# Optimization experiments

Measured on AMD Instinct MI355X. Metric: run time of the kernel, lower is better.

The kernel has to match this reference:

```python
import jax, jax.numpy as jnp
import numpy as np

B, S, I, H = 128, 512, 256, 512

def setup_inputs() -> dict:
    key = jax.random.key(0)
    ks = jax.random.split(key, 8)
    s_wd = 1.0 / np.sqrt(H)
    s_u = 1.0 / np.sqrt(I)
    return {
        "inputs": jax.random.normal(ks[0], (B, S, I), dtype=jnp.float32),
        "timestamps": jax.random.uniform(ks[1], (B, S), dtype=jnp.float32),
        "W_all_w": jax.random.uniform(ks[2], (4 * H, H), minval=-s_wd, maxval=s_wd, dtype=jnp.float32),
        "W_all_b": jax.random.uniform(ks[3], (4 * H,), minval=-s_wd, maxval=s_wd, dtype=jnp.float32),
        "U_all_w": jax.random.uniform(ks[4], (4 * H, I), minval=-s_u, maxval=s_u, dtype=jnp.float32),
        "U_all_b": jax.random.uniform(ks[5], (4 * H,), minval=-s_u, maxval=s_u, dtype=jnp.float32),
        "W_d_w": jax.random.uniform(ks[6], (H, H), minval=-s_wd, maxval=s_wd, dtype=jnp.float32),
        "W_d_b": jax.random.uniform(ks[7], (H,), minval=-s_wd, maxval=s_wd, dtype=jnp.float32),
    }

def reference(inputs, timestamps, W_all_w, W_all_b, U_all_w, U_all_b, W_d_w, W_d_b):
    b, seq, _ = inputs.shape
    hdim = W_d_w.shape[0]
    # Precompute input projection for all steps: [b, s, 4H] -> scan over [s, b, 4H]
    u_all = jnp.einsum("bsi,gi->bsg", inputs, U_all_w) + U_all_b
    u_seq = jnp.swapaxes(u_all, 0, 1)          # [s, b, 4H]
    t_seq = jnp.swapaxes(timestamps, 0, 1)     # [s, b]

    def step(carry, xs):
        h, c = carry
        u, t = xs
        c_s1 = jnp.tanh(c @ W_d_w.T + W_d_b)
        c_adj = c - c_s1 + c_s1 * t[:, None]   # c_l + c_s2
        outs = h @ W_all_w.T + W_all_b + u
        f, i, o, c_tmp = jnp.split(outs, 4, axis=1)
        f = jax.nn.sigmoid(f)
        i = jax.nn.sigmoid(i)
        o = jax.nn.sigmoid(o)
        c_tmp = jax.nn.sigmoid(c_tmp)
        c_new = f * c_adj + i * c_tmp
        h_new = o * jnp.tanh(c_new)
        return (h_new, c_new), h_new

    h0 = jnp.zeros((b, hdim), dtype=inputs.dtype)
    c0 = jnp.zeros((b, hdim), dtype=inputs.dtype)
    _, outputs = jax.lax.scan(step, (h0, c0), (u_seq, t_seq))
    return jnp.swapaxes(outputs, 0, 1)         # [b, s, H]
```

## Files before the change

kernel.cpp:

```cpp
#include <hip/hip_runtime.h>


#define Bq 128
#define Sq 512
#define Iq 256
#define Hq 512

typedef __bf16  bf16x8  __attribute__((ext_vector_type(8)));
typedef float   floatx4 __attribute__((ext_vector_type(4)));
typedef unsigned short ushort;
typedef ushort  ushort8 __attribute__((ext_vector_type(8)));
typedef unsigned long long u64;

__device__ __forceinline__ ushort f2bf(float f) {
    union { float f; unsigned u; } v; v.f = f;
    unsigned r = v.u + 0x7fffu + ((v.u >> 16) & 1u);
    return (ushort)(r >> 16);
}

__device__ __forceinline__ float sigm(float x) { return 1.f / (1.f + __expf(-x)); }
__device__ __forceinline__ float tanh_fast(float x) {
    float e = __expf(2.f * x);
    return 1.f - 2.f / (e + 1.f);
}

__device__ __forceinline__ bf16x8 pack8(float4 a, float4 b) {
    ushort8 v;
    v[0] = f2bf(a.x); v[1] = f2bf(a.y); v[2] = f2bf(a.z); v[3] = f2bf(a.w);
    v[4] = f2bf(b.x); v[5] = f2bf(b.y); v[6] = f2bf(b.z); v[7] = f2bf(b.w);
    return __builtin_bit_cast(bf16x8, v);
}

__global__ __launch_bounds__(256, 1) void lstm_kernel(
    const float* __restrict__ xin,
    const float* __restrict__ tsp,
    const float* __restrict__ Ww, const float* __restrict__ Wb,
    const float* __restrict__ Uw, const float* __restrict__ Ub,
    const float* __restrict__ Dw, const float* __restrict__ Db,
    unsigned* __restrict__ hcbuf,
    unsigned* __restrict__ slots,
    float* __restrict__ out)
{
    __shared__ ushort h_s[16 * 520];
    __shared__ ushort c_s[16 * 520];
    __shared__ ushort x_s[16 * 264];
    __shared__ float  gb[4 * 256];
    __shared__ float  gd[4 * 256];
    __shared__ float  bias_g[64];
    __shared__ float  bias_d[16];

    const int tid  = threadIdx.x;
    const int lane = tid & 63;
    const int wv   = tid >> 6;
    const int n    = lane & 15;
    const int quad = lane >> 4;
    const int gq   = blockIdx.x & 7;
    const int s    = blockIdx.x >> 3;
    const int jj   = s * 16;

    bf16x8 bW[16], bU[8], bD[4];
    {
        const int Rw = wv * Hq + jj + n;
        #pragma unroll
        for (int kk = 0; kk < 16; ++kk) {
            const float4* p = (const float4*)(Ww + (size_t)Rw * Hq + kk * 32 + quad * 8);
            bW[kk] = pack8(p[0], p[1]);
        }
        #pragma unroll
        for (int kk = 0; kk < 8; ++kk) {
            const float4* p = (const float4*)(Uw + (size_t)Rw * Iq + kk * 32 + quad * 8);
            bU[kk] = pack8(p[0], p[1]);
        }
        const int Rd = jj + n;
        #pragma unroll
        for (int kq = 0; kq < 4; ++kq) {
            const float4* p = (const float4*)(Dw + (size_t)Rd * Hq + (wv * 4 + kq) * 32 + quad * 8);
            bD[kq] = pack8(p[0], p[1]);
        }
    }
    if (tid < 64)
        bias_g[tid] = Wb[(tid >> 4) * Hq + jj + (tid & 15)] + Ub[(tid >> 4) * Hq + jj + (tid & 15)];
    if (tid >= 64 && tid < 80)
        bias_d[tid - 64] = Db[jj + (tid - 64)];
    __syncthreads();

    float c_reg = 0.f;
    const int b = tid >> 4, j = tid & 15;
    const int grow = gq * 16 + b;

    const ushort* hp = &h_s[n * 520 + quad * 8];
    const ushort* cp = &c_s[n * 520 + quad * 8];
    const ushort* xp = &x_s[n * 264 + quad * 8];

    unsigned* myslot = &slots[gq * 64 + s];
    unsigned* pollp  = &slots[gq * 64 + (lane & 31)];

    const float* xbase = xin + ((size_t)(gq * 16 + (tid >> 4)) * Sq) * Iq + (tid & 15) * 16;
    float4 x0, x1, x2, x3;
    {
        const float4* p = (const float4*)xbase;
        x0 = p[0]; x1 = p[1]; x2 = p[2]; x3 = p[3];
    }

    for (int t = 0; t < Sq; ++t) {
        float tt = tsp[(size_t)grow * Sq + t];

        const u64* hsrc = (const u64*)(hcbuf + ((size_t)(t & 1) * 8 + gq) * 8192);
        const u64* csrc = hsrc + 2048;
        u64 hv[8], cv[8];
        #pragma unroll
        for (int k = 0; k < 8; ++k)
            hv[k] = __hip_atomic_load(hsrc + k * 256 + tid, __ATOMIC_RELAXED, __HIP_MEMORY_SCOPE_AGENT);
        #pragma unroll
        for (int k = 0; k < 8; ++k)
            cv[k] = __hip_atomic_load(csrc + k * 256 + tid, __ATOMIC_RELAXED, __HIP_MEMORY_SCOPE_AGENT);

        {
            bf16x8 v0 = pack8(x0, x1);
            bf16x8 v1 = pack8(x2, x3);
            ushort* xd = &x_s[(tid >> 4) * 264 + (tid & 15) * 16];
            *(bf16x8*)xd       = v0;
            *(bf16x8*)(xd + 8) = v1;
        }

        #pragma unroll
        for (int k = 0; k < 8; ++k) {
            const int m   = k * 256 + tid;
            const int row = m >> 7;
            const int col = (m << 2) & 511;
            *(u64*)&h_s[row * 520 + col] = hv[k];
            *(u64*)&c_s[row * 520 + col] = cv[k];
        }
        __syncthreads();

        floatx4 accW = {0.f, 0.f, 0.f, 0.f};
        floatx4 accU = {0.f, 0.f, 0.f, 0.f};
        floatx4 accD = {0.f, 0.f, 0.f, 0.f};
        #pragma unroll
        for (int kk = 0; kk < 16; ++kk) {
            bf16x8 ah = *(const bf16x8*)(hp + kk * 32);
            accW = __builtin_amdgcn_mfma_f32_16x16x32_bf16(ah, bW[kk], accW, 0, 0, 0);
            if (kk < 8) {
                bf16x8 ax = *(const bf16x8*)(xp + kk * 32);
                accU = __builtin_amdgcn_mfma_f32_16x16x32_bf16(ax, bU[kk], accU, 0, 0, 0);
            }
            if ((kk >> 2) == wv) {
                bf16x8 ac = *(const bf16x8*)(cp + kk * 32);
                accD = __builtin_amdgcn_mfma_f32_16x16x32_bf16(ac, bD[kk & 3], accD, 0, 0, 0);
            }
        }
        accW += accU;

        #pragma unroll
        for (int r2 = 0; r2 < 4; ++r2) {
            gb[wv * 256 + (quad * 4 + r2) * 16 + n] = accW[r2];
            gd[wv * 256 + (quad * 4 + r2) * 16 + n] = accD[r2];
        }
        __syncthreads();

        float pf = gb[tid]       + bias_g[j];
        float pi = gb[256 + tid] + bias_g[16 + j];
        float po = gb[512 + tid] + bias_g[32 + j];
        float pc = gb[768 + tid] + bias_g[48 + j];
        float csum = gd[tid] + gd[256 + tid] + gd[512 + tid] + gd[768 + tid] + bias_d[j];
        float c_s1  = tanh_fast(csum);
        float c_adj = c_reg - c_s1 + c_s1 * tt;
        float fg = sigm(pf), ig = sigm(pi), og = sigm(po), cg = sigm(pc);
        float c_new = fg * c_adj + ig * cg;
        float h_new = og * tanh_fast(c_new);
        c_reg = c_new;

        out[((size_t)grow * Sq + t) * Hq + jj + j] = h_new;

        {
            unsigned my    = ((unsigned)f2bf(c_new) << 16) | (unsigned)f2bf(h_new);
            unsigned other = __shfl_xor(my, 1);
            unsigned* dst  = hcbuf + ((size_t)((t + 1) & 1) * 8 + gq) * 8192;
            const int pidx = b * 256 + ((jj + j) >> 1);
            if ((j & 1) == 0) {
                unsigned hpair = ((other & 0xFFFFu) << 16) | (my & 0xFFFFu);
                __hip_atomic_store(dst + pidx, hpair, __ATOMIC_RELAXED, __HIP_MEMORY_SCOPE_AGENT);
            } else {
                unsigned cpair = (my & 0xFFFF0000u) | (other >> 16);
                __hip_atomic_store(dst + 4096 + pidx, cpair, __ATOMIC_RELAXED, __HIP_MEMORY_SCOPE_AGENT);
            }
        }
        __syncthreads();

        if (t < Sq - 1) {
            const unsigned tgt = (unsigned)(t + 1);
            if (tid == 0)
                __hip_atomic_store(myslot, tgt, __ATOMIC_RELAXED, __HIP_MEMORY_SCOPE_AGENT);

            {
                const float4* p = (const float4*)(xbase + (size_t)(t + 1) * Iq);
                x0 = p[0]; x1 = p[1]; x2 = p[2]; x3 = p[3];
            }

            if (wv == 0) {
                for (;;) {
                    unsigned vv = __hip_atomic_load(pollp, __ATOMIC_RELAXED, __HIP_MEMORY_SCOPE_AGENT);
                    if (__all(vv >= tgt)) break;
                    __builtin_amdgcn_s_sleep(2);
                }
            }
            __syncthreads();
        }
    }
}

extern "C" void kernel_launch(void* const* d_in, const int* in_sizes, int n_in,
                              void* d_out, int out_size, void* d_ws, size_t ws_size,
                              hipStream_t stream) {
    const float* inputs = (const float*)d_in[0];
    const float* tsp    = (const float*)d_in[1];
    const float* Ww     = (const float*)d_in[2];
    const float* Wb     = (const float*)d_in[3];
    const float* Uw     = (const float*)d_in[4];
    const float* Ub     = (const float*)d_in[5];
    const float* Dw     = (const float*)d_in[6];
    const float* Db     = (const float*)d_in[7];
    float* out = (float*)d_out;

    char* ws = (char*)d_ws;
    unsigned* hcbuf = (unsigned*)ws;
    unsigned* slots = (unsigned*)(ws + 524288);

    hipMemsetAsync(ws, 0, 262144, stream);
    hipMemsetAsync(ws + 524288, 0, 2048, stream);

    lstm_kernel<<<dim3(256), dim3(256), 0, stream>>>(
        inputs, tsp, Ww, Wb, Uw, Ub, Dw, Db, hcbuf, slots, out);
}
```

Baseline: 1.816 ms.

## Use XCC-local sc0 loads/stores for h/c exchange when group shares an XCD

At startup each block records its XCC id, and the 32 blocks of a batch group check whether they all sit on the same XCD. If they do, the per-step h/c state exchange uses global loads and stores with only the sc0 cache bit instead of agent-scope atomics, so traffic can stay in the shared L2 rather than going further out. An explicit s_waitcnt is added before the shared-memory writes. The fast path relies on the hardware scheduler placing a group on one XCD; the startup handshake adds a small cost, and the sc0 coherence assumptions are subtle.

Measured after the change: 1.854 ms. +2.1%, slower.

```diff
diff --git a/kernel.cpp b/kernel.cpp
--- a/kernel.cpp
+++ b/kernel.cpp
@@ -29,6 +29,15 @@
     v[0] = f2bf(a.x); v[1] = f2bf(a.y); v[2] = f2bf(a.z); v[3] = f2bf(a.w);
     v[4] = f2bf(b.x); v[5] = f2bf(b.y); v[6] = f2bf(b.z); v[7] = f2bf(b.w);
     return __builtin_bit_cast(bf16x8, v);
+}
+
+__device__ __forceinline__ u64 ld_sc0_b64(const u64* p) {
+    u64 r;
+    asm volatile("global_load_dwordx2 %0, %1, off sc0" : "=v"(r) : "v"(p) : "memory");
+    return r;
+}
+__device__ __forceinline__ void st_sc0_b32(unsigned* p, unsigned v) {
+    asm volatile("global_store_dword %0, %1, off sc0" :: "v"(p), "v"(v) : "memory");
 }
 
 __global__ __launch_bounds__(256, 1) void lstm_kernel(
@@ -48,6 +57,7 @@
     __shared__ float  gd[4 * 256];
     __shared__ float  bias_g[64];
     __shared__ float  bias_d[16];
+    __shared__ int    fastflag_s;
 
     const int tid  = threadIdx.x;
     const int lane = tid & 63;
@@ -82,7 +92,28 @@
         bias_g[tid] = Wb[(tid >> 4) * Hq + jj + (tid & 15)] + Ub[(tid >> 4) * Hq + jj + (tid & 15)];
     if (tid >= 64 && tid < 80)
         bias_d[tid - 64] = Db[jj + (tid - 64)];
-    __syncthreads();
+
+    {
+        int xcc;
+        asm volatile("s_getreg_b32 %0, hwreg(HW_REG_XCC_ID)" : "=s"(xcc));
+        if (tid == 0)
+            __hip_atomic_store(&slots[gq * 64 + 32 + s], (unsigned)(xcc + 1),
+                               __ATOMIC_RELAXED, __HIP_MEMORY_SCOPE_AGENT);
+        if (wv == 0) {
+            unsigned vv;
+            for (;;) {
+                vv = __hip_atomic_load(&slots[gq * 64 + 32 + (lane & 31)],
+                                       __ATOMIC_RELAXED, __HIP_MEMORY_SCOPE_AGENT);
+                if (__all(vv != 0)) break;
+                __builtin_amdgcn_s_sleep(2);
+            }
+            unsigned f0 = __shfl(vv, 0);
+            int alleq = __all(vv == f0);
+            if (lane == 0) fastflag_s = alleq;
+        }
+        __syncthreads();
+    }
+    const bool fastpath = (fastflag_s != 0);
 
     float c_reg = 0.f;
     const int b = tid >> 4, j = tid & 15;
@@ -108,12 +139,19 @@
         const u64* hsrc = (const u64*)(hcbuf + ((size_t)(t & 1) * 8 + gq) * 8192);
         const u64* csrc = hsrc + 2048;
         u64 hv[8], cv[8];
-        #pragma unroll
-        for (int k = 0; k < 8; ++k)
-            hv[k] = __hip_atomic_load(hsrc + k * 256 + tid, __ATOMIC_RELAXED, __HIP_MEMORY_SCOPE_AGENT);
-        #pragma unroll
-        for (int k = 0; k < 8; ++k)
-            cv[k] = __hip_atomic_load(csrc + k * 256 + tid, __ATOMIC_RELAXED, __HIP_MEMORY_SCOPE_AGENT);
+        if (fastpath) {
+            #pragma unroll
+            for (int k = 0; k < 8; ++k) hv[k] = ld_sc0_b64(hsrc + k * 256 + tid);
+            #pragma unroll
+            for (int k = 0; k < 8; ++k) cv[k] = ld_sc0_b64(csrc + k * 256 + tid);
+        } else {
+            #pragma unroll
+            for (int k = 0; k < 8; ++k)
+                hv[k] = __hip_atomic_load(hsrc + k * 256 + tid, __ATOMIC_RELAXED, __HIP_MEMORY_SCOPE_AGENT);
+            #pragma unroll
+            for (int k = 0; k < 8; ++k)
+                cv[k] = __hip_atomic_load(csrc + k * 256 + tid, __ATOMIC_RELAXED, __HIP_MEMORY_SCOPE_AGENT);
+        }
 
         {
             bf16x8 v0 = pack8(x0, x1);
@@ -121,6 +159,11 @@
             ushort* xd = &x_s[(tid >> 4) * 264 + (tid & 15) * 16];
             *(bf16x8*)xd       = v0;
             *(bf16x8*)(xd + 8) = v1;
+        }
+
+        if (fastpath) {
+            asm volatile("s_waitcnt vmcnt(0)" ::: "memory");
+            __builtin_amdgcn_sched_barrier(0);
         }
 
         #pragma unroll
@@ -177,13 +220,18 @@
             unsigned other = __shfl_xor(my, 1);
             unsigned* dst  = hcbuf + ((size_t)((t + 1) & 1) * 8 + gq) * 8192;
             const int pidx = b * 256 + ((jj + j) >> 1);
+            unsigned val; unsigned* ptr;
             if ((j & 1) == 0) {
-                unsigned hpair = ((other & 0xFFFFu) << 16) | (my & 0xFFFFu);
-                __hip_atomic_store(dst + pidx, hpair, __ATOMIC_RELAXED, __HIP_MEMORY_SCOPE_AGENT);
+                val = ((other & 0xFFFFu) << 16) | (my & 0xFFFFu);
+                ptr = dst + pidx;
             } else {
-                unsigned cpair = (my & 0xFFFF0000u) | (other >> 16);
-                __hip_atomic_store(dst + 4096 + pidx, cpair, __ATOMIC_RELAXED, __HIP_MEMORY_SCOPE_AGENT);
-            }
+                val = (my & 0xFFFF0000u) | (other >> 16);
+                ptr = dst + 4096 + pidx;
+            }
+            if (fastpath)
+                st_sc0_b32(ptr, val);
+            else
+                __hip_atomic_store(ptr, val, __ATOMIC_RELAXED, __HIP_MEMORY_SCOPE_AGENT);
         }
         __syncthreads();
 
```

## Split each batch group into two half-batches and ping-pong them to hide grid-sync latency

Applied to the files above, without the earlier changes.

Each block's 16 batch rows become two 8-row halves (A and B) that take turns through the recurrence. Each half has its own flags and h/c exchange buffers, so the wait on the other half's grid-wide flags overlaps the current half's MFMA and gate work. The inter-block barrier latency is meant to be hidden behind useful compute. In exchange the MFMA work per step doubles, since each pass still runs full 16-row tiles and discards half of them. Gate math now runs on only two waves while the other waves poll, and raw s_barrier plus waitcnt asm add correctness risk.

Result: slower. 2.636 ms (+45.2%).

```diff
diff --git a/kernel.cpp b/kernel.cpp
--- a/kernel.cpp
+++ b/kernel.cpp
@@ -29,6 +29,12 @@
     v[0] = f2bf(a.x); v[1] = f2bf(a.y); v[2] = f2bf(a.z); v[3] = f2bf(a.w);
     v[4] = f2bf(b.x); v[5] = f2bf(b.y); v[6] = f2bf(b.z); v[7] = f2bf(b.w);
     return __builtin_bit_cast(bf16x8, v);
+}
+
+__device__ __forceinline__ void block_bar() {
+    asm volatile("" ::: "memory");
+    __builtin_amdgcn_s_barrier();
+    asm volatile("" ::: "memory");
 }
 
 __global__ __launch_bounds__(256, 1) void lstm_kernel(
@@ -44,8 +50,8 @@
     __shared__ ushort h_s[16 * 520];
     __shared__ ushort c_s[16 * 520];
     __shared__ ushort x_s[16 * 264];
-    __shared__ float  gb[4 * 256];
-    __shared__ float  gd[4 * 256];
+    __shared__ float  gb[4 * 128];
+    __shared__ float  gd[4 * 128];
     __shared__ float  bias_g[64];
     __shared__ float  bias_d[16];
 
@@ -54,7 +60,7 @@
     const int wv   = tid >> 6;
     const int n    = lane & 15;
     const int quad = lane >> 4;
-    const int gq   = blockIdx.x & 7;
+    const int q    = blockIdx.x & 7;
     const int s    = blockIdx.x >> 3;
     const int jj   = s * 16;
 
@@ -84,127 +90,237 @@
         bias_d[tid - 64] = Db[jj + (tid - 64)];
     __syncthreads();
 
-    float c_reg = 0.f;
-    const int b = tid >> 4, j = tid & 15;
-    const int grow = gq * 16 + b;
+    const int gt    = tid & 127;
+    const int gjrow = gt >> 4;
+    const int gj    = tid & 15;
+
+    float cA = 0.f, cB = 0.f, hA = 0.f, hB = 0.f;
 
     const ushort* hp = &h_s[n * 520 + quad * 8];
     const ushort* cp = &c_s[n * 520 + quad * 8];
     const ushort* xp = &x_s[n * 264 + quad * 8];
 
-    unsigned* myslot = &slots[gq * 64 + s];
-    unsigned* pollp  = &slots[gq * 64 + (lane & 31)];
-
-    const float* xbase = xin + ((size_t)(gq * 16 + (tid >> 4)) * Sq) * Iq + (tid & 15) * 16;
-    float4 x0, x1, x2, x3;
+    unsigned* flagA = &slots[q * 128 + s];
+    unsigned* flagB = &slots[q * 128 + 64 + s];
+    const unsigned* pollA = &slots[q * 128 + (lane & 31)];
+    const unsigned* pollB = &slots[q * 128 + 64 + (lane & 31)];
+
+    const int xrow = tid >> 5;
+    const int xcol = (tid & 31) * 8;
+    const float* xbaseA = xin + ((size_t)(q * 16 + xrow) * Sq) * Iq + xcol;
+    const float* xbaseB = xin + ((size_t)(q * 16 + 8 + xrow) * Sq) * Iq + xcol;
+    ushort* xdstA = &x_s[xrow * 264 + xcol];
+    ushort* xdstB = &x_s[(8 + xrow) * 264 + xcol];
+
+    float4 xA0, xA1, xB0, xB1;
+    { const float4* p = (const float4*)xbaseA; xA0 = p[0]; xA1 = p[1]; }
+    { const float4* p = (const float4*)xbaseB; xB0 = p[0]; xB1 = p[1]; }
+
     {
-        const float4* p = (const float4*)xbase;
-        x0 = p[0]; x1 = p[1]; x2 = p[2]; x3 = p[3];
-    }
-
-    for (int t = 0; t < Sq; ++t) {
-        float tt = tsp[(size_t)grow * Sq + t];
-
-        const u64* hsrc = (const u64*)(hcbuf + ((size_t)(t & 1) * 8 + gq) * 8192);
-        const u64* csrc = hsrc + 2048;
-        u64 hv[8], cv[8];
-        #pragma unroll
-        for (int k = 0; k < 8; ++k)
-            hv[k] = __hip_atomic_load(hsrc + k * 256 + tid, __ATOMIC_RELAXED, __HIP_MEMORY_SCOPE_AGENT);
-        #pragma unroll
-        for (int k = 0; k < 8; ++k)
-            cv[k] = __hip_atomic_load(csrc + k * 256 + tid, __ATOMIC_RELAXED, __HIP_MEMORY_SCOPE_AGENT);
-
-        {
-            bf16x8 v0 = pack8(x0, x1);
-            bf16x8 v1 = pack8(x2, x3);
-            ushort* xd = &x_s[(tid >> 4) * 264 + (tid & 15) * 16];
-            *(bf16x8*)xd       = v0;
-            *(bf16x8*)(xd + 8) = v1;
-        }
-
-        #pragma unroll
-        for (int k = 0; k < 8; ++k) {
+        const u64* hc = (const u64*)(hcbuf + (size_t)(q * 2 + 0) * 4096);
+        u64 hv[4], cv[4];
+        #pragma unroll
+        for (int k = 0; k < 4; ++k)
+            hv[k] = __hip_atomic_load(hc + k * 256 + tid, __ATOMIC_RELAXED, __HIP_MEMORY_SCOPE_AGENT);
+        #pragma unroll
+        for (int k = 0; k < 4; ++k)
+            cv[k] = __hip_atomic_load(hc + 1024 + k * 256 + tid, __ATOMIC_RELAXED, __HIP_MEMORY_SCOPE_AGENT);
+        *(bf16x8*)xdstA = pack8(xA0, xA1);
+        #pragma unroll
+        for (int k = 0; k < 4; ++k) {
             const int m   = k * 256 + tid;
             const int row = m >> 7;
-            const int col = (m << 2) & 511;
+            const int col = (4 * m) & 511;
             *(u64*)&h_s[row * 520 + col] = hv[k];
             *(u64*)&c_s[row * 520 + col] = cv[k];
         }
+    }
+    __syncthreads();
+
+    for (int t = 0; t < Sq; ++t) {
+        float ttA = 0.f, ttB = 0.f;
+        if (tid >= 128) {
+            ttA = tsp[(size_t)(q * 16 + gjrow) * Sq + t];
+            ttB = tsp[(size_t)(q * 16 + 8 + gjrow) * Sq + t];
+        }
+
+        {
+            floatx4 accW = {0.f,0.f,0.f,0.f}, accU = {0.f,0.f,0.f,0.f}, accD = {0.f,0.f,0.f,0.f};
+            #pragma unroll
+            for (int kk = 0; kk < 16; ++kk) {
+                bf16x8 ah = *(const bf16x8*)(hp + kk * 32);
+                accW = __builtin_amdgcn_mfma_f32_16x16x32_bf16(ah, bW[kk], accW, 0, 0, 0);
+                if (kk < 8) {
+                    bf16x8 ax = *(const bf16x8*)(xp + kk * 32);
+                    accU = __builtin_amdgcn_mfma_f32_16x16x32_bf16(ax, bU[kk], accU, 0, 0, 0);
+                }
+                if ((kk >> 2) == wv) {
+                    bf16x8 ac = *(const bf16x8*)(cp + kk * 32);
+                    accD = __builtin_amdgcn_mfma_f32_16x16x32_bf16(ac, bD[kk & 3], accD, 0, 0, 0);
+                }
+            }
+            accW += accU;
+            if (quad < 2) {
+                #pragma unroll
+                for (int r2 = 0; r2 < 4; ++r2) {
+                    gb[wv * 128 + (quad * 4 + r2) * 16 + n] = accW[r2];
+                    gd[wv * 128 + (quad * 4 + r2) * 16 + n] = accD[r2];
+                }
+            }
+        }
         __syncthreads();
 
-        floatx4 accW = {0.f, 0.f, 0.f, 0.f};
-        floatx4 accU = {0.f, 0.f, 0.f, 0.f};
-        floatx4 accD = {0.f, 0.f, 0.f, 0.f};
-        #pragma unroll
-        for (int kk = 0; kk < 16; ++kk) {
-            bf16x8 ah = *(const bf16x8*)(hp + kk * 32);
-            accW = __builtin_amdgcn_mfma_f32_16x16x32_bf16(ah, bW[kk], accW, 0, 0, 0);
-            if (kk < 8) {
-                bf16x8 ax = *(const bf16x8*)(xp + kk * 32);
-                accU = __builtin_amdgcn_mfma_f32_16x16x32_bf16(ax, bU[kk], accU, 0, 0, 0);
-            }
-            if ((kk >> 2) == wv) {
-                bf16x8 ac = *(const bf16x8*)(cp + kk * 32);
-                accD = __builtin_amdgcn_mfma_f32_16x16x32_bf16(ac, bD[kk & 3], accD, 0, 0, 0);
-            }
-        }
-        accW += accU;
-
-        #pragma unroll
-        for (int r2 = 0; r2 < 4; ++r2) {
-            gb[wv * 256 + (quad * 4 + r2) * 16 + n] = accW[r2];
-            gd[wv * 256 + (quad * 4 + r2) * 16 + n] = accD[r2];
+        if (tid >= 128) {
+            float pf = gb[gt]       + bias_g[gj];
+            float pi = gb[128 + gt] + bias_g[16 + gj];
+            float po = gb[256 + gt] + bias_g[32 + gj];
+            float pc = gb[384 + gt] + bias_g[48 + gj];
+            float csum = gd[gt] + gd[128 + gt] + gd[256 + gt] + gd[384 + gt] + bias_d[gj];
+            float c_s1  = tanh_fast(csum);
+            float c_adj = cA - c_s1 + c_s1 * ttA;
+            float fg = sigm(pf), ig = sigm(pi), og = sigm(po), cg = sigm(pc);
+            float c_new = fg * c_adj + ig * cg;
+            hA = og * tanh_fast(c_new);
+            cA = c_new;
+            unsigned my    = ((unsigned)f2bf(c_new) << 16) | (unsigned)f2bf(hA);
+            unsigned other = __shfl_xor(my, 1);
+            unsigned* dst  = hcbuf + ((size_t)((t + 1) & 1) * 16 + q * 2 + 0) * 4096;
+            const int pidx = gjrow * 256 + ((jj + gj) >> 1);
+            if ((gj & 1) == 0)
+                __hip_atomic_store(dst + pidx, ((other & 0xFFFFu) << 16) | (my & 0xFFFFu),
+                                   __ATOMIC_RELAXED, __HIP_MEMORY_SCOPE_AGENT);
+            else
+                __hip_atomic_store(dst + 2048 + pidx, (my & 0xFFFF0000u) | (other >> 16),
+                                   __ATOMIC_RELAXED, __HIP_MEMORY_SCOPE_AGENT);
+            asm volatile("s_waitcnt vmcnt(0)" ::: "memory");
+        } else if (wv == 0 && t > 0) {
+            const unsigned tgt = (unsigned)t;
+            for (;;) {
+                unsigned vv = __hip_atomic_load(pollB, __ATOMIC_RELAXED, __HIP_MEMORY_SCOPE_AGENT);
+                if (__all(vv >= tgt)) break;
+                __builtin_amdgcn_s_sleep(2);
+            }
+        }
+        block_bar();
+        if (tid == 0)
+            __hip_atomic_store(flagA, (unsigned)(t + 1), __ATOMIC_RELAXED, __HIP_MEMORY_SCOPE_AGENT);
+
+        {
+            const u64* hc = (const u64*)(hcbuf + ((size_t)(t & 1) * 16 + q * 2 + 1) * 4096);
+            u64 hv[4], cv[4];
+            #pragma unroll
+            for (int k = 0; k < 4; ++k)
+                hv[k] = __hip_atomic_load(hc + k * 256 + tid, __ATOMIC_RELAXED, __HIP_MEMORY_SCOPE_AGENT);
+            #pragma unroll
+            for (int k = 0; k < 4; ++k)
+                cv[k] = __hip_atomic_load(hc + 1024 + k * 256 + tid, __ATOMIC_RELAXED, __HIP_MEMORY_SCOPE_AGENT);
+            if (tid >= 128)
+                out[((size_t)(q * 16 + gjrow) * Sq + t) * Hq + jj + gj] = hA;
+            if (t < Sq - 1) {
+                const float4* p = (const float4*)(xbaseA + (size_t)(t + 1) * Iq);
+                xA0 = p[0]; xA1 = p[1];
+            }
+            *(bf16x8*)xdstB = pack8(xB0, xB1);
+            #pragma unroll
+            for (int k = 0; k < 4; ++k) {
+                const int m   = k * 256 + tid;
+                const int row = 8 + (m >> 7);
+                const int col = (4 * m) & 511;
+                *(u64*)&h_s[row * 520 + col] = hv[k];
+                *(u64*)&c_s[row * 520 + col] = cv[k];
+            }
         }
         __syncthreads();
 
-        float pf = gb[tid]       + bias_g[j];
-        float pi = gb[256 + tid] + bias_g[16 + j];
-        float po = gb[512 + tid] + bias_g[32 + j];
-        float pc = gb[768 + tid] + bias_g[48 + j];
-        float csum = gd[tid] + gd[256 + tid] + gd[512 + tid] + gd[768 + tid] + bias_d[j];
-        float c_s1  = tanh_fast(csum);
-        float c_adj = c_reg - c_s1 + c_s1 * tt;
-        float fg = sigm(pf), ig = sigm(pi), og = sigm(po), cg = sigm(pc);
-        float c_new = fg * c_adj + ig * cg;
-        float h_new = og * tanh_fast(c_new);
-        c_reg = c_new;
-
-        out[((size_t)grow * Sq + t) * Hq + jj + j] = h_new;
-
         {
-            unsigned my    = ((unsigned)f2bf(c_new) << 16) | (unsigned)f2bf(h_new);
+            floatx4 accW = {0.f,0.f,0.f,0.f}, accU = {0.f,0.f,0.f,0.f}, accD = {0.f,0.f,0.f,0.f};
+            #pragma unroll
+            for (int kk = 0; kk < 16; ++kk) {
+                bf16x8 ah = *(const bf16x8*)(hp + kk * 32);
+                accW = __builtin_amdgcn_mfma_f32_16x16x32_bf16(ah, bW[kk], accW, 0, 0, 0);
+                if (kk < 8) {
+                    bf16x8 ax = *(const bf16x8*)(xp + kk * 32);
+                    accU = __builtin_amdgcn_mfma_f32_16x16x32_bf16(ax, bU[kk], accU, 0, 0, 0);
+                }
+                if ((kk >> 2) == wv) {
+                    bf16x8 ac = *(const bf16x8*)(cp + kk * 32);
+                    accD = __builtin_amdgcn_mfma_f32_16x16x32_bf16(ac, bD[kk & 3], accD, 0, 0, 0);
+                }
+            }
+            accW += accU;
+            if (quad >= 2) {
+                #pragma unroll
+                for (int r2 = 0; r2 < 4; ++r2) {
+                    gb[wv * 128 + ((quad - 2) * 4 + r2) * 16 + n] = accW[r2];
+                    gd[wv * 128 + ((quad - 2) * 4 + r2) * 16 + n] = accD[r2];
+                }
+            }
+        }
+        __syncthreads();
+
+        if (tid >= 128) {
+            float pf = gb[gt]       + bias_g[gj];
+            float pi = gb[128 + gt] + bias_g[16 + gj];
+            float po = gb[256 + gt] + bias_g[32 + gj];
+            float pc = gb[384 + gt] + bias_g[48 + gj];
+            float csum = gd[gt] + gd[128 + gt] + gd[256 + gt] + gd[384 + gt] + bias_d[gj];
+            float c_s1  = tanh_fast(csum);
+            float c_adj = cB - c_s1 + c_s1 * ttB;
+            float fg = sigm(pf), ig = sigm(pi), og = sigm(po), cg = sigm(pc);
+            float c_new = fg * c_adj + ig * cg;
+            hB = og * tanh_fast(c_new);
+            cB = c_new;
+            unsigned my    = ((unsigned)f2bf(c_new) << 16) | (unsigned)f2bf(hB);
             unsigned other = __shfl_xor(my, 1);
-            unsigned* dst  = hcbuf + ((size_t)((t + 1) & 1) * 8 + gq) * 8192;
-            const int pidx = b * 256 + ((jj + j) >> 1);
-            if ((j & 1) == 0) {
-                unsigned hpair = ((other & 0xFFFFu) << 16) | (my & 0xFFFFu);
-                __hip_atomic_store(dst + pidx, hpair, __ATOMIC_RELAXED, __HIP_MEMORY_SCOPE_AGENT);
-            } else {
-                unsigned cpair = (my & 0xFFFF0000u) | (other >> 16);
-                __hip_atomic_store(dst + 4096 + pidx, cpair, __ATOMIC_RELAXED, __HIP_MEMORY_SCOPE_AGENT);
-            }
-        }
-        __syncthreads();
+            unsigned* dst  = hcbuf + ((size_t)((t + 1) & 1) * 16 + q * 2 + 1) * 4096;
+            const int pidx = gjrow * 256 + ((jj + gj) >> 1);
+            if ((gj & 1) == 0)
+                __hip_atomic_store(dst + pidx, ((other & 0xFFFFu) << 16) | (my & 0xFFFFu),
+                                   __ATOMIC_RELAXED, __HIP_MEMORY_SCOPE_AGENT);
+            else
+                __hip_atomic_store(dst + 2048 + pidx, (my & 0xFFFF0000u) | (other >> 16),
+                                   __ATOMIC_RELAXED, __HIP_MEMORY_SCOPE_AGENT);
+            asm volatile("s_waitcnt vmcnt(0)" ::: "memory");
+        } else if (wv == 0 && t < Sq - 1) {
+            const unsigned tgt = (unsigned)(t + 1);
+            for (;;) {
+                unsigned vv = __hip_atomic_load(pollA, __ATOMIC_RELAXED, __HIP_MEMORY_SCOPE_AGENT);
+                if (__all(vv >= tgt)) break;
+                __builtin_amdgcn_s_sleep(2);
+            }
+        }
+        block_bar();
+        if (tid == 0)
+            __hip_atomic_store(flagB, (unsigned)(t + 1), __ATOMIC_RELAXED, __HIP_MEMORY_SCOPE_AGENT);
 
         if (t < Sq - 1) {
-            const unsigned tgt = (unsigned)(t + 1);
-            if (tid == 0)
-                __hip_atomic_store(myslot, tgt, __ATOMIC_RELAXED, __HIP_MEMORY_SCOPE_AGENT);
-
+            const u64* hc = (const u64*)(hcbuf + ((size_t)((t + 1) & 1) * 16 + q * 2 + 0) * 4096);
+            u64 hv[4], cv[4];
+            #pragma unroll
+            for (int k = 0; k < 4; ++k)
+                hv[k] = __hip_atomic_load(hc + k * 256 + tid, __ATOMIC_RELAXED, __HIP_MEMORY_SCOPE_AGENT);
+            #pragma unroll
+            for (int k = 0; k < 4; ++k)
+                cv[k] = __hip_atomic_load(hc + 1024 + k * 256 + tid, __ATOMIC_RELAXED, __HIP_MEMORY_SCOPE_AGENT);
+            if (tid >= 128)
+                out[((size_t)(q * 16 + 8 + gjrow) * Sq + t) * Hq + jj + gj] = hB;
             {
-                const float4* p = (const float4*)(xbase + (size_t)(t + 1) * Iq);
-                x0 = p[0]; x1 = p[1]; x2 = p[2]; x3 = p[3];
-            }
-
-            if (wv == 0) {
-                for (;;) {
-                    unsigned vv = __hip_atomic_load(pollp, __ATOMIC_RELAXED, __HIP_MEMORY_SCOPE_AGENT);
-                    if (__all(vv >= tgt)) break;
-                    __builtin_amdgcn_s_sleep(2);
-                }
+                const float4* p = (const float4*)(xbaseB + (size_t)(t + 1) * Iq);
+                xB0 = p[0]; xB1 = p[1];
+            }
+            *(bf16x8*)xdstA = pack8(xA0, xA1);
+            #pragma unroll
+            for (int k = 0; k < 4; ++k) {
+                const int m   = k * 256 + tid;
+                const int row = m >> 7;
+                const int col = (4 * m) & 511;
+                *(u64*)&h_s[row * 520 + col] = hv[k];
+                *(u64*)&c_s[row * 520 + col] = cv[k];
             }
             __syncthreads();
+        } else {
+            if (tid >= 128)
+                out[((size_t)(q * 16 + 8 + gjrow) * Sq + t) * Hq + jj + gj] = hB;
         }
     }
 }
@@ -227,7 +343,7 @@
     unsigned* slots = (unsigned*)(ws + 524288);
 
     hipMemsetAsync(ws, 0, 262144, stream);
-    hipMemsetAsync(ws + 524288, 0, 2048, stream);
+    hipMemsetAsync(ws + 524288, 0, 4096, stream);
 
     lstm_kernel<<<dim3(256), dim3(256), 0, stream>>>(
         inputs, tsp, Ww, Wb, Uw, Ub, Dw, Db, hcbuf, slots, out);
```
